# Optimization experiments

Measured on AMD Instinct MI355X. Metric: run time of the kernel, lower is better.

## Reference

```python
import jax, jax.numpy as jnp
import numpy as np

TAU = 0.5
BS, NQ, NT = 8, 8192, 512


def _lsa_rect(cost):
    """Rectangular linear sum assignment (shortest augmenting path, as in
    scipy.optimize.linear_sum_assignment). cost: (R, C) with R <= C.
    Returns col4row: for each row r, the assigned column."""
    R, C = cost.shape
    u = np.zeros(R, np.float64)
    v = np.zeros(C, np.float64)
    path = np.full(C, -1, np.int64)
    col4row = np.full(R, -1, np.int64)
    row4col = np.full(C, -1, np.int64)
    for cur_row in range(R):
        min_val = 0.0
        i = cur_row
        remaining = np.ones(C, bool)
        SR = np.zeros(R, bool)
        shortest = np.full(C, np.inf)
        sink = -1
        while sink == -1:
            SR[i] = True
            rem = np.nonzero(remaining)[0]
            r = min_val + cost[i, rem] - u[i] - v[rem]
            better = r < shortest[rem]
            upd = rem[better]
            shortest[upd] = r[better]
            path[upd] = i
            k = rem[np.argmin(shortest[rem])]
            min_val = shortest[k]
            remaining[k] = False
            if row4col[k] == -1:
                sink = k
            else:
                i = row4col[k]
        # dual updates
        u[cur_row] += min_val
        sr = np.nonzero(SR)[0]
        sr = sr[sr != cur_row]
        u[sr] += min_val - shortest[col4row[sr]]
        sc = ~remaining
        v[sc] -= min_val - shortest[sc]
        # augment along the alternating path
        j = sink
        while True:
            i = path[j]
            row4col[j] = i
            col4row[i], j = j, col4row[i]
            if i == cur_row:
                break
    return col4row


def setup_inputs() -> dict:
    key = jax.random.key(0)
    k1, k2, k3 = jax.random.split(key, 3)
    pred_logits = jax.random.normal(k1, (BS, NQ, 1), jnp.float32)
    # points live in a [0, 512)^2 image-coordinate box
    pred_points = jax.random.uniform(k2, (BS, NQ, 2), jnp.float32) * 512.0
    tgt_points = jax.random.uniform(k3, (BS, NT, 2), jnp.float32) * 512.0
    return {"pred_logits": pred_logits, "pred_points": pred_points,
            "tgt_points": tgt_points}


def reference(pred_logits, pred_points, tgt_points):
    # out_prob: [bs, N];  cost_class = 1 - sigmoid(logit)
    prob = jax.nn.sigmoid(pred_logits)[..., 0]
    # pairwise L2 distances [bs, N, M] (torch.cdist p=2)
    diff = pred_points[:, :, None, :] - tgt_points[:, None, :, :]
    dists = jnp.sqrt(jnp.sum(diff * diff, axis=-1))
    C = TAU * dists + (1.0 - prob)[:, :, None]
    # Hungarian assignment per sample (host-side, same math as scipy).
    Cn = np.asarray(jax.device_get(C), dtype=np.float64)
    rows, cols = [], []
    for b in range(Cn.shape[0]):
        # N > M: solve on the transpose (M rows, N cols), like scipy does.
        assigned = _lsa_rect(Cn[b].T)  # per target -> query index
        order = np.argsort(assigned)   # scipy returns row_ind sorted
        rows.append(assigned[order])
        cols.append(order)
    row_ind = jnp.asarray(np.stack(rows), jnp.int64)
    col_ind = jnp.asarray(np.stack(cols), jnp.int64)
    return C, row_ind, col_ind
```

## Files before the change

### kernel.cpp

```cpp
#include <hip/hip_runtime.h>
#include <math.h>

#define BS 8
#define NQ 8192
#define NT 512
#define NTHR 512
#define CHUNKS 16
#define NW (NTHR / 64)
#define NG 16
#define MAXL (NT + 2)
#define QCAP 4608
#define KMASK 0xFFFFFFFFFFFFE000ull
#define CFB 240

#define DINF (__builtin_inf())

typedef float vf4 __attribute__((ext_vector_type(4)));

__device__ __forceinline__ float cost_f32(float qx, float qy, float cl, float tx, float ty) {
    float dx = __fsub_rn(qx, tx);
    float dy = __fsub_rn(qy, ty);
    float d2 = __fadd_rn(__fmul_rn(dx, dx), __fmul_rn(dy, dy));
    float d  = __fsqrt_rn(d2);
    return __fadd_rn(__fmul_rn(0.5f, d), cl);
}

__device__ __forceinline__ float cls_f32(float x) {
    float s;
    if (x >= 0.0f) { float e = expf(-x); s = 1.0f / (1.0f + e); }
    else           { float e = expf(x);  s = e / (1.0f + e); }
    return __fsub_rn(1.0f, s);
}

__device__ __forceinline__ unsigned long long pack_key(double v, int idx) {
    double c = fmax(v, 0.0);
    return (((unsigned long long)__double_as_longlong(c)) & KMASK)
         | (unsigned long long)((unsigned)idx & 0x1FFFu);
}
__device__ __forceinline__ double key_val(unsigned long long k) {
    return __longlong_as_double((long long)(k & KMASK));
}

__device__ __forceinline__ void merge2(
    float a0, float a1, int ai0, int ai1, float am,
    float b0, float b1, int bi0, int bi1, float bm,
    float& o0, float& o1, int& oi0, int& oi1, float& om) {
    float s3;
    const bool bWins = (b0 < a0) || (b0 == a0 && bi0 < ai0);
    if (!bWins) {
        o0 = a0; oi0 = ai0;
        const bool a1W = (a1 < b0) || (a1 == b0 && ai1 < bi0);
        if (a1W) { o1 = a1; oi1 = ai1; s3 = b0; }
        else     { o1 = b0; oi1 = bi0; s3 = fminf(a1, b1); }
    } else {
        o0 = b0; oi0 = bi0;
        const bool b1W = (b1 < a0) || (b1 == a0 && bi1 < ai0);
        if (b1W) { o1 = b1; oi1 = bi1; s3 = a0; }
        else     { o1 = a0; oi1 = ai0; s3 = fminf(b1, a1); }
    }
    om = fminf(fminf(am, bm), s3);
}

__global__ __launch_bounds__(1024) void cand_kernel(
    const float* __restrict__ logits,
    const float* __restrict__ pred_points,
    const float* __restrict__ tgt_points,
    float* __restrict__ cls_out,
    float* __restrict__ u0, int* __restrict__ jm, float* __restrict__ bnd,
    float* __restrict__ ccost, unsigned short* __restrict__ cidx) {
    extern __shared__ char sm[];
    float2* pd = (float2*)sm;
    float*  cl = (float*)(pd + NQ);

    const int tid = threadIdx.x;
    const int b   = blockIdx.x >> 5;

    const float4* p4 = (const float4*)(pred_points + (size_t)b * NQ * 2);
    for (int t = tid; t < NQ / 2; t += 1024) ((float4*)pd)[t] = p4[t];
    for (int t = tid; t < NQ; t += 1024) cl[t] = cls_f32(logits[b * NQ + t]);
    __syncthreads();
    if ((blockIdx.x & 31) == 0) {
        for (int t = tid; t < NQ; t += 1024) cls_out[b * NQ + t] = cl[t];
    }

    const int w = tid >> 6, lane = tid & 63;
    const int i = (blockIdx.x & 31) * 16 + w;
    const int g = b * NT + i;
    const float tx = tgt_points[g * 2 + 0];
    const float ty = tgt_points[g * 2 + 1];

    float A0 = DINF, A1 = DINF, Am = DINF; int Ai0 = 0, Ai1 = 0;
    float B0 = DINF, B1 = DINF, Bm = DINF; int Bi0 = 0, Bi1 = 0;
    float C0 = DINF, C1 = DINF, Cm = DINF; int Ci0 = 0, Ci1 = 0;
    float D0 = DINF, D1 = DINF, Dm = DINF; int Di0 = 0, Di1 = 0;
    for (int k = 0; k < NQ / 256; ++k) {
        const int c = k * 256 + 4 * lane;
        const float4 p01 = ((const float4*)pd)[(c >> 1) + 0];
        const float4 p23 = ((const float4*)pd)[(c >> 1) + 1];
        const float4 c4  = ((const float4*)cl)[c >> 2];
        const float v0 = cost_f32(p01.x, p01.y, c4.x, tx, ty);
        const float v1 = cost_f32(p01.z, p01.w, c4.y, tx, ty);
        const float v2 = cost_f32(p23.x, p23.y, c4.z, tx, ty);
        const float v3 = cost_f32(p23.z, p23.w, c4.w, tx, ty);
        if (v0 < A1) { Am = A1; if (v0 < A0) { A1 = A0; Ai1 = Ai0; A0 = v0; Ai0 = c; } else { A1 = v0; Ai1 = c; } }
        else Am = fminf(Am, v0);
        if (v1 < B1) { Bm = B1; if (v1 < B0) { B1 = B0; Bi1 = Bi0; B0 = v1; Bi0 = c + 1; } else { B1 = v1; Bi1 = c + 1; } }
        else Bm = fminf(Bm, v1);
        if (v2 < C1) { Cm = C1; if (v2 < C0) { C1 = C0; Ci1 = Ci0; C0 = v2; Ci0 = c + 2; } else { C1 = v2; Ci1 = c + 2; } }
        else Cm = fminf(Cm, v2);
        if (v3 < D1) { Dm = D1; if (v3 < D0) { D1 = D0; Di1 = Di0; D0 = v3; Di0 = c + 3; } else { D1 = v3; Di1 = c + 3; } }
        else Dm = fminf(Dm, v3);
    }
    float ab0, ab1, abm; int abi0, abi1;
    float cd0, cd1, cdm; int cdi0, cdi1;
    float t0v, t1v, bb0; int t0i, t1i;
    merge2(A0, A1, Ai0, Ai1, Am, B0, B1, Bi0, Bi1, Bm, ab0, ab1, abi0, abi1, abm);
    merge2(C0, C1, Ci0, Ci1, Cm, D0, D1, Di0, Di1, Dm, cd0, cd1, cdi0, cdi1, cdm);
    merge2(ab0, ab1, abi0, abi1, abm, cd0, cd1, cdi0, cdi1, cdm, t0v, t1v, t0i, t1i, bb0);

    ((float2*)(ccost + ((size_t)g << 7)))[lane] = make_float2(t0v, t1v);
    ((ushort2*)(cidx + ((size_t)g << 7)))[lane] =
        make_ushort2((unsigned short)t0i, (unsigned short)t1i);
    float bv = t0v; int bc = t0i; float bb = bb0;
    for (int off = 32; off > 0; off >>= 1) {
        float ov = __shfl_down(bv, off, 64);
        int   oc = __shfl_down(bc, off, 64);
        float ob = __shfl_down(bb, off, 64);
        if (ov < bv || (ov == bv && oc < bc)) { bv = ov; bc = oc; }
        bb = fminf(bb, ob);
    }
    if (lane == 0) { u0[g] = bv; jm[g] = bc; bnd[g] = bb; }
}

__global__ __launch_bounds__(NTHR, 1) void fused_kernel(
    const float* __restrict__ pred_points,
    const float* __restrict__ tgt_points,
    const float* __restrict__ cls,
    const float* __restrict__ u0,
    const int* __restrict__ jm,
    const float* __restrict__ bnd,
    const float* __restrict__ ccost,
    const unsigned short* __restrict__ cidx,
    float* __restrict__ C,
    float* __restrict__ out_rows,
    float* __restrict__ out_cols) {
    const int tid = threadIdx.x;

    if (blockIdx.x >= BS) {
        const int cfid = blockIdx.x - BS;
        const int ngrp = BS * NQ / 16;
        const int g32  = tid & 31;
        for (int grp = cfid; grp < ngrp; grp += CFB) {
            const int bq = (grp << 4) + (tid >> 5);
            const int b  = bq >> 13;
            const float2 q = ((const float2*)pred_points)[bq];
            const float clv = cls[bq];
            const float* tb = tgt_points + b * NT * 2;
#pragma unroll
            for (int s = 0; s < 4; ++s) {
                const int t = g32 * 4 + s * 128;
                float4 A  = *(const float4*)(tb + t * 2);
                float4 Bv = *(const float4*)(tb + t * 2 + 4);
                vf4 r;
                r.x = cost_f32(q.x, q.y, clv, A.x,  A.y);
                r.y = cost_f32(q.x, q.y, clv, A.z,  A.w);
                r.z = cost_f32(q.x, q.y, clv, Bv.x, Bv.y);
                r.w = cost_f32(q.x, q.y, clv, Bv.z, Bv.w);
                __builtin_nontemporal_store(r, (vf4*)(C + (size_t)bq * NT + t));
            }
        }
        return;
    }

    const int b = blockIdx.x;
    extern __shared__ char smem[];
    double* v_s       = (double*)smem;
    double* u_s       = v_s + NQ;
    double* l_minv    = u_s + NT;
    double* l_v       = l_minv + MAXL;
    double* a_m2      = l_v + MAXL;
    unsigned long long* p_k = (unsigned long long*)(a_m2 + NG);
    float*  tg        = (float*)(p_k + 2 * NW);
    float*  bnd_s     = tg + NT * 2;
    float*  a_c       = bnd_s + NT;
    int*    s_int     = (int*)(a_c + NG);
    int*    a_j       = s_int + 4;
    short*  path_s    = (short*)(a_j + NG);
    short*  row4col_s = path_s + NQ;
    short*  col4row_s = row4col_s + NQ;
    short*  jm_s      = col4row_s + NT;
    short*  dflag     = jm_s + NT;
    short*  sap_s     = dflag + NT;
    short*  l_k       = sap_s + NT;
    short*  l_r       = l_k + MAXL;
    short*  queue_s   = l_r + MAXL;

    for (int c = tid; c < NQ; c += NTHR) { row4col_s[c] = -1; v_s[c] = 0.0; }
    for (int r = tid; r < NT; r += NTHR) {
        col4row_s[r] = -1;
        u_s[r]   = (double)u0[b * NT + r];
        jm_s[r]  = (short)jm[b * NT + r];
        bnd_s[r] = bnd[b * NT + r];
    }
    for (int t = tid; t < NT * 2; t += NTHR) tg[t] = tgt_points[b * NT * 2 + t];

    float  qx[CHUNKS], qy[CHUNKS], cl[CHUNKS];
    double vv[CHUNKS], sh[CHUNKS];
#pragma unroll
    for (int j = 0; j < CHUNKS; ++j) {
        int c = j * NTHR + tid;
        qx[j] = pred_points[(b * NQ + c) * 2 + 0];
        qy[j] = pred_points[(b * NQ + c) * 2 + 1];
        cl[j] = cls[b * NQ + c];
    }
    __syncthreads();

    {
        const int r = tid;
        const short jmr = jm_s[r];
        int conflict = 0;
        for (int r2 = 0; r2 < r; ++r2) conflict |= (jm_s[r2] == jmr) ? 1 : 0;
        dflag[r] = (short)conflict;
        if (!conflict) { col4row_s[r] = jmr; row4col_s[jmr] = (short)r; }
        __syncthreads();
        int rank = 0;
        for (int r2 = 0; r2 < r; ++r2) rank += dflag[r2];
        if (conflict) queue_s[rank] = (short)r;
        if (r == NT - 1) s_int[0] = rank + conflict;
        __syncthreads();
    }

    int head = 0, tail = s_int[0], nsap = 0;
    {
        const int tail0 = tail;
        int rcap = tail0 + 48; if (rcap > 192) rcap = 192;
        const int grp = tid >> 5, gl = tid & 31;
        int rounds = 0;
        while (head < tail && rounds < rcap) {
            const int nrows = (tail - head < NG) ? (tail - head) : NG;
            if (grp < nrows) {
                const int row = queue_s[head + grp];
                const int g = (b << 9) + row;
                const float4  cc = ((const float4*)(ccost + ((size_t)g << 7)))[gl];
                const ushort4 ci = ((const ushort4*)(cidx + ((size_t)g << 7)))[gl];
                const unsigned long long q0 = pack_key((double)cc.x - v_s[ci.x], ci.x);
                const unsigned long long q1 = pack_key((double)cc.y - v_s[ci.y], ci.y);
                const unsigned long long q2 = pack_key((double)cc.z - v_s[ci.z], ci.z);
                const unsigned long long q3 = pack_key((double)cc.w - v_s[ci.w], ci.w);
                unsigned long long ka = q0 < q1 ? q0 : q1, kb = q0 < q1 ? q1 : q0;
                unsigned long long kc = q2 < q3 ? q2 : q3, kd = q2 < q3 ? q3 : q2;
                unsigned long long k1  = ka < kc ? ka : kc;
                unsigned long long t2_ = ka < kc ? kc : ka;
                unsigned long long t3_ = kb < kd ? kb : kd;
                unsigned long long m2b = (t2_ < t3_ ? t2_ : t3_) & KMASK;
                for (int m = 16; m > 0; m >>= 1) {
                    unsigned long long ok1 = __shfl_xor(k1, m, 32);
                    unsigned long long om2 = __shfl_xor(m2b, m, 32);
                    unsigned long long lo  = (ok1 < k1) ? ok1 : k1;
                    unsigned long long hiv = ((ok1 < k1) ? k1 : ok1) & KMASK;
                    k1 = lo;
                    if (om2 < m2b) m2b = om2;
                    if (hiv < m2b) m2b = hiv;
                }
                const double m2d = key_val(m2b);
                if (q0 == k1) a_c[grp] = cc.x;
                if (q1 == k1) a_c[grp] = cc.y;
                if (q2 == k1) a_c[grp] = cc.z;
                if (q3 == k1) a_c[grp] = cc.w;
                if (gl == 0) {
                    a_m2[grp] = m2d;
                    a_j[grp]  = (m2d < (double)bnd_s[row]) ? (int)(k1 & 0x1FFFull) : -1;
                }
            }
            __syncthreads();
            int   cjv[NG], kov[NG], rowv[NG], act[NG];
            double m2v[NG]; float cwv[NG];
#pragma unroll
            for (int e = 0; e < NG; ++e) {
                cjv[e] = -1; act[e] = 0;
                if (e < nrows) {
                    rowv[e] = queue_s[head + e];
                    const int j1 = a_j[e];
                    if (j1 < 0) { act[e] = 3; }
                    else {
                        int dup = 0;
#pragma unroll
                        for (int x = 0; x < NG; ++x)
                            if (x < e) dup |= (cjv[x] == j1) ? 1 : 0;
                        if (dup) { act[e] = 2; }
                        else {
                            act[e] = 1; cjv[e] = j1;
                            kov[e] = row4col_s[j1];
                            m2v[e] = a_m2[e]; cwv[e] = a_c[e];
                        }
                    }
                }
            }
            __syncthreads();
            {
                int t2 = tail, ns = nsap;
#pragma unroll
                for (int e = 0; e < NG; ++e) {
                    if (act[e] == 1) {
                        const int j1 = cjv[e];
                        row4col_s[j1]     = (short)rowv[e];
                        col4row_s[rowv[e]] = (short)j1;
                        u_s[rowv[e]] = m2v[e];
                        const double nv = (double)cwv[e] - m2v[e];
                        if (nv < v_s[j1]) v_s[j1] = nv;
                        if (kov[e] >= 0) {
                            col4row_s[kov[e]] = -1;
                            queue_s[t2++] = (short)kov[e];
                        }
                    } else if (act[e] == 2) {
                        queue_s[t2++] = (short)rowv[e];
                    } else if (act[e] == 3) {
                        sap_s[ns++] = (short)rowv[e];
                    }
                }
                head += nrows; tail = t2; nsap = ns;
            }
            ++rounds;
        }
        for (int e = head; e < tail; ++e) sap_s[nsap++] = queue_s[e];
    }
    __syncthreads();

#pragma unroll
    for (int j = 0; j < CHUNKS; ++j) vv[j] = v_s[j * NTHR + tid];

    const int NL = nsap;
    for (int di = 0; di < NL; ++di) {
        const int cur_row = sap_s[di];
#pragma unroll
        for (int j = 0; j < CHUNKS; ++j) sh[j] = DINF;
        int    i    = cur_row;
        double minv = 0.0;
        int    len  = 0;
        int    sink = -1;

        for (;;) {
            const double w  = minv - u_s[i];
            const float  tx = tg[i * 2 + 0];
            const float  ty = tg[i * 2 + 1];

            double best = DINF;
            int bestc = NQ;
#pragma unroll
            for (int j = 0; j < CHUNKS; ++j) {
                const int c = j * NTHR + tid;
                float  cf = cost_f32(qx[j], qy[j], cl[j], tx, ty);
                double rr = (w + (double)cf) - vv[j];
                if (rr < sh[j]) { sh[j] = rr; path_s[c] = (short)i; }
                if (sh[j] < best) { best = sh[j]; bestc = c; }
            }
            unsigned long long bkey = pack_key(best, bestc);
            for (int off = 32; off > 0; off >>= 1) {
                unsigned long long ok = __shfl_down(bkey, off, 64);
                if (ok < bkey) bkey = ok;
            }
            const int par = len & 1;
            if ((tid & 63) == 0) p_k[par * NW + (tid >> 6)] = bkey;
            __syncthreads();
            bkey = p_k[par * NW + (tid & (NW - 1))];
            for (int m = NW >> 1; m > 0; m >>= 1) {
                unsigned long long ok = __shfl_xor(bkey, m, 64);
                if (ok < bkey) bkey = ok;
            }
            minv = key_val(bkey);
            const int k  = (int)(bkey & 0x1FFFull);
            const int rk = row4col_s[k];
            if ((k & (NTHR - 1)) == tid) {
                const int jj = k >> 9;
#pragma unroll
                for (int j = 0; j < CHUNKS; ++j)
                    if (j == jj) { l_v[len] = vv[j]; vv[j] = -DINF; sh[j] = DINF; }
            }
            if (tid == 0) { l_k[len] = (short)k; l_minv[len] = minv; l_r[len] = (short)rk; }
            ++len;
            if (rk < 0) { sink = k; break; }
            i = rk;
        }
        __syncthreads();

        const int L = len;
        for (int e = tid; e < L; e += NTHR) {
            const int rk2 = l_r[e];
            if (rk2 >= 0) u_s[rk2] += minv - l_minv[e];
        }
        if (tid == 0) u_s[cur_row] += minv;
        for (int e = 0; e < L; ++e) {
            const int k2 = l_k[e];
            if ((k2 & (NTHR - 1)) == tid) {
                const int jj = k2 >> 9;
                const double nv = l_v[e] - (minv - l_minv[e]);
#pragma unroll
                for (int j = 0; j < CHUNKS; ++j)
                    if (j == jj) vv[j] = nv;
            }
        }
        if (tid == 0) {
            int j = sink;
            for (;;) {
                const int ii = path_s[j];
                row4col_s[j] = (short)ii;
                const int t = col4row_s[ii];
                col4row_s[ii] = (short)j;
                j = t;
                if (ii == cur_row) break;
            }
        }
        __syncthreads();
    }

    for (int r = tid; r < NT; r += NTHR) {
        const int q = col4row_s[r];
        int rank = 0;
        for (int r2 = 0; r2 < NT; ++r2) rank += (col4row_s[r2] < q) ? 1 : 0;
        out_rows[b * NT + rank] = (float)q;
        out_cols[b * NT + rank] = (float)r;
    }
}

extern "C" void kernel_launch(void* const* d_in, const int* in_sizes, int n_in,
                              void* d_out, int out_size, void* d_ws, size_t ws_size,
                              hipStream_t stream) {
    const float* logits = (const float*)d_in[0];
    const float* pred   = (const float*)d_in[1];
    const float* tgt    = (const float*)d_in[2];

    float* out  = (float*)d_out;
    float* C    = out;
    float* orow = out + (size_t)BS * NQ * NT;
    float* ocol = orow + (size_t)BS * NT;

    char*  ws    = (char*)d_ws;
    float* cls   = (float*)ws;
    float* u0    = (float*)(ws + 262144);
    float* bndp  = (float*)(ws + 278528);
    int*   jmn   = (int*)(ws + 294912);
    float* ccost = (float*)(ws + 311296);
    unsigned short* cidx = (unsigned short*)(ws + 311296 + 2097152);

    const size_t smem_cand  = 98304;
    const size_t smem_fused = 132608;

    cand_kernel<<<BS * 32, 1024, smem_cand, stream>>>(
        logits, pred, tgt, cls, u0, jmn, bndp, ccost, cidx);
    fused_kernel<<<BS + CFB, NTHR, smem_fused, stream>>>(
        pred, tgt, cls, u0, jmn, bndp, ccost, cidx, C, orow, ocol);
}
```

Before: 88.55 us.

## Use atomicMin+ballot conflict detection and prefetch next auction round's candidate rows

Replaces the O(NT) serial per-thread scans for duplicate-column detection and conflict ranking with an atomicMin over a shared scratch array (aliased onto v_s) plus a wave-ballot prefix count. It also prefetches the next round's per-row candidate cost and index vectors from global memory before the barrier, so that load latency overlaps the per-round bookkeeping. The scratch aliasing requires v_s to be re-zeroed after the conflict pass, and the prefetch adds register pressure. The prefetched data is reused only when a group's next row matches.

```diff
diff --git a/kernel.cpp b/kernel.cpp
--- a/kernel.cpp
+++ b/kernel.cpp
@@ -185,17 +185,17 @@
     float*  a_c       = bnd_s + NT;
     int*    s_int     = (int*)(a_c + NG);
     int*    a_j       = s_int + 4;
-    short*  path_s    = (short*)(a_j + NG);
+    int*    wcnt      = a_j + NG;
+    short*  path_s    = (short*)(wcnt + NW);
     short*  row4col_s = path_s + NQ;
     short*  col4row_s = row4col_s + NQ;
     short*  jm_s      = col4row_s + NT;
-    short*  dflag     = jm_s + NT;
-    short*  sap_s     = dflag + NT;
+    short*  sap_s     = jm_s + NT;
     short*  l_k       = sap_s + NT;
     short*  l_r       = l_k + MAXL;
     short*  queue_s   = l_r + MAXL;
 
-    for (int c = tid; c < NQ; c += NTHR) { row4col_s[c] = -1; v_s[c] = 0.0; }
+    for (int c = tid; c < NQ; c += NTHR) row4col_s[c] = -1;
     for (int r = tid; r < NT; r += NTHR) {
         col4row_s[r] = -1;
         u_s[r]   = (double)u0[b * NT + r];
@@ -216,17 +216,27 @@
     __syncthreads();
 
     {
+        int* scratch = (int*)v_s;
         const int r = tid;
-        const short jmr = jm_s[r];
-        int conflict = 0;
-        for (int r2 = 0; r2 < r; ++r2) conflict |= (jm_s[r2] == jmr) ? 1 : 0;
-        dflag[r] = (short)conflict;
-        if (!conflict) { col4row_s[r] = jmr; row4col_s[jmr] = (short)r; }
-        __syncthreads();
-        int rank = 0;
-        for (int r2 = 0; r2 < r; ++r2) rank += dflag[r2];
+        const int jmr = jm_s[r];
+        scratch[jmr] = 0x7FFFFFFF;
+        __syncthreads();
+        atomicMin(&scratch[jmr], r);
+        __syncthreads();
+        const bool conflict = (scratch[jmr] != r);
+        if (!conflict) { col4row_s[r] = (short)jmr; row4col_s[jmr] = (short)r; }
+        const unsigned long long bal = __ballot(conflict);
+        const int lane = tid & 63, w = tid >> 6;
+        if (lane == 0) wcnt[w] = __popcll(bal);
+        __syncthreads();
+        int pre = 0, tot = 0;
+        for (int x = 0; x < NW; ++x) { if (x < w) pre += wcnt[x]; tot += wcnt[x]; }
+        const int rank = pre + __popcll(bal & ((1ull << lane) - 1ull));
         if (conflict) queue_s[rank] = (short)r;
-        if (r == NT - 1) s_int[0] = rank + conflict;
+        if (tid == 0) s_int[0] = 0;
+        __syncthreads();
+        for (int c = tid; c < NQ; c += NTHR) v_s[c] = 0.0;
+        if (tid == 0) s_int[0] = tot;
         __syncthreads();
     }
 
@@ -236,13 +246,18 @@
         int rcap = tail0 + 48; if (rcap > 192) rcap = 192;
         const int grp = tid >> 5, gl = tid & 31;
         int rounds = 0;
+        int pf_row = -1; float4 pf_cc; ushort4 pf_ci;
         while (head < tail && rounds < rcap) {
             const int nrows = (tail - head < NG) ? (tail - head) : NG;
             if (grp < nrows) {
                 const int row = queue_s[head + grp];
-                const int g = (b << 9) + row;
-                const float4  cc = ((const float4*)(ccost + ((size_t)g << 7)))[gl];
-                const ushort4 ci = ((const ushort4*)(cidx + ((size_t)g << 7)))[gl];
+                float4 cc; ushort4 ci;
+                if (row == pf_row) { cc = pf_cc; ci = pf_ci; }
+                else {
+                    const int g = (b << 9) + row;
+                    cc = ((const float4*)(ccost + ((size_t)g << 7)))[gl];
+                    ci = ((const ushort4*)(cidx + ((size_t)g << 7)))[gl];
+                }
                 const unsigned long long q0 = pack_key((double)cc.x - v_s[ci.x], ci.x);
                 const unsigned long long q1 = pack_key((double)cc.y - v_s[ci.y], ci.y);
                 const unsigned long long q2 = pack_key((double)cc.z - v_s[ci.z], ci.z);
@@ -272,6 +287,16 @@
                     a_j[grp]  = (m2d < (double)bnd_s[row]) ? (int)(k1 & 0x1FFFull) : -1;
                 }
             }
+            {
+                const int np = head + nrows + grp;
+                if (np < tail) {
+                    const int prow = queue_s[np];
+                    const int pg = (b << 9) + prow;
+                    pf_cc = ((const float4*)(ccost + ((size_t)pg << 7)))[gl];
+                    pf_ci = ((const ushort4*)(cidx + ((size_t)pg << 7)))[gl];
+                    pf_row = prow;
+                } else pf_row = -1;
+            }
             __syncthreads();
             int   cjv[NG], kov[NG], rowv[NG], act[NG];
             double m2v[NG]; float cwv[NG];
```

Measured after the change: 80.86 us. -8.7%, faster.
